# Kernel optimization log

Measured on AMD Instinct MI355X. Metric: run time of the kernel, lower is better.

## Reference

```python
import jax, jax.numpy as jnp
import numpy as np

T, R, H, DK = 2, 3, 4, 32
IN_DIM, OUT_DIM = 128, 128
N = 50000
E = 400000
RELS = [(0, 1), (1, 0), (1, 1)]  # (src_type, dst_type) per relation


def setup_inputs() -> dict:
    key = jax.random.key(0)
    ks = jax.random.split(key, 24)
    lin_scale = float(np.sqrt(2.0 / (IN_DIM + OUT_DIM)))
    att_scale = float(np.sqrt(2.0 / (DK + DK)))
    inp = {
        'h0': jax.random.normal(ks[0], (N, IN_DIM), jnp.float32),
        'h1': jax.random.normal(ks[1], (N, IN_DIM), jnp.float32),
        'Wk': jax.random.normal(ks[2], (T, IN_DIM, OUT_DIM), jnp.float32) * lin_scale,
        'bk': jnp.zeros((T, OUT_DIM), jnp.float32),
        'Wq': jax.random.normal(ks[3], (T, IN_DIM, OUT_DIM), jnp.float32) * lin_scale,
        'bq': jnp.zeros((T, OUT_DIM), jnp.float32),
        'Wv': jax.random.normal(ks[4], (T, IN_DIM, OUT_DIM), jnp.float32) * lin_scale,
        'bv': jnp.zeros((T, OUT_DIM), jnp.float32),
        'Wa': jax.random.normal(ks[5], (T, OUT_DIM, OUT_DIM), jnp.float32) * lin_scale,
        'ba': jnp.zeros((T, OUT_DIM), jnp.float32),
        'rel_att': jax.random.normal(ks[6], (R, H, DK, DK), jnp.float32) * att_scale,
        'rel_msg': jax.random.normal(ks[7], (R, H, DK, DK), jnp.float32) * att_scale,
        'rel_pri': jnp.ones((R, H), jnp.float32),
        'skip': jnp.ones((T,), jnp.float32),
        'src0': jax.random.randint(ks[8], (E,), 0, N, jnp.int32),
        'dst0': jax.random.randint(ks[9], (E,), 0, N, jnp.int32),
        'src1': jax.random.randint(ks[10], (E,), 0, N, jnp.int32),
        'dst1': jax.random.randint(ks[11], (E,), 0, N, jnp.int32),
        'src2': jax.random.randint(ks[12], (E,), 0, N, jnp.int32),
        'dst2': jax.random.randint(ks[13], (E,), 0, N, jnp.int32),
    }
    return inp


def _hgt_forward(h0, h1, Wk, bk, Wq, bq, Wv, bv, Wa, ba,
                 rel_att, rel_msg, rel_pri, skip, edges):
    sqrt_dk = np.sqrt(DK).astype(np.float32)
    hs = [h0, h1]
    # per-type k/q/v projections, reshaped to [N, H, DK]
    k_all = [(hs[t] @ Wk[t] + bk[t]).reshape(-1, H, DK) for t in range(T)]
    q_all = [(hs[t] @ Wq[t] + bq[t]).reshape(-1, H, DK) for t in range(T)]
    v_all = [(hs[t] @ Wv[t] + bv[t]).reshape(-1, H, DK) for t in range(T)]
    agg = {0: [], 1: []}
    for r, (s, d) in enumerate(RELS):
        src, dst = edges[r]
        k = jnp.einsum('nhi,hij->nhj', k_all[s], rel_att[r])
        v = jnp.einsum('nhi,hij->nhj', v_all[s], rel_msg[r])
        q = q_all[d]
        # edge-wise dot-product attention score [E, H]
        score = jnp.einsum('ehd,ehd->eh', q[dst], k[src]) * rel_pri[r] / sqrt_dk
        # edge softmax normalized by destination node
        m = jax.ops.segment_max(score, dst, num_segments=N)
        e = jnp.exp(score - m[dst])
        z = jax.ops.segment_sum(e, dst, num_segments=N)
        a = e / z[dst]
        msg = v[src] * a[..., None]  # [E, H, DK]
        agg[d].append(jax.ops.segment_sum(msg, dst, num_segments=N))
    outs = []
    for t in range(T):
        tmean = agg[t][0]
        for extra in agg[t][1:]:
            tmean = tmean + extra
        tmean = tmean / jnp.float32(len(agg[t]))  # cross_reducer='mean'
        tt = tmean.reshape(-1, OUT_DIM)
        trans = tt @ Wa[t] + ba[t]  # dropout p=0 -> identity
        alpha = jax.nn.sigmoid(skip[t])
        outs.append(trans * alpha + hs[t] * (1.0 - alpha))
    return jnp.stack(outs)  # [T, N, OUT_DIM]


def reference(h0, h1, Wk, bk, Wq, bq, Wv, bv, Wa, ba,
              rel_att, rel_msg, rel_pri, skip,
              src0, dst0, src1, dst1, src2, dst2):
    edges = [(src0, dst0), (src1, dst1), (src2, dst2)]
    return _hgt_forward(h0, h1, Wk, bk, Wq, bq, Wv, bv, Wa, ba,
                        rel_att, rel_msg, rel_pri, skip, edges)
```

## Files before the change

kernel.cpp:

```cpp
#include <hip/hip_runtime.h>
#include <hip/hip_bf16.h>
#include <math.h>


#define NN 50000
#define EE 400000
#define CAP 40
#define NBKT 196
#define SLICE 40

typedef __bf16 bf16x8 __attribute__((ext_vector_type(8)));
typedef float floatx4 __attribute__((ext_vector_type(4)));
typedef _Float16 h2 __attribute__((ext_vector_type(2)));

#if __has_builtin(__builtin_amdgcn_exp2f)
#define EXP2F(x) __builtin_amdgcn_exp2f(x)
#else
#define EXP2F(x) exp2f(x)
#endif

__device__ __forceinline__ h2 u_to_h2(unsigned int u) {
    union { unsigned int u; h2 h; } x; x.u = u; return x.h;
}

__device__ __forceinline__ float dot2f(h2 a, h2 b, float c) {
#if __has_builtin(__builtin_amdgcn_fdot2)
    return __builtin_amdgcn_fdot2(a, b, c, false);
#else
    return fmaf((float)a.x, (float)b.x, fmaf((float)a.y, (float)b.y, c));
#endif
}

__device__ __forceinline__ float xor1_add(float x) {
#if __has_builtin(__builtin_amdgcn_mov_dpp)
    int y = __builtin_amdgcn_mov_dpp(__float_as_int(x), 0xB1, 0xf, 0xf, true);
    return x + __int_as_float(y);
#else
    return x + __shfl_xor(x, 1);
#endif
}
__device__ __forceinline__ float xor2_add(float x) {
#if __has_builtin(__builtin_amdgcn_mov_dpp)
    int y = __builtin_amdgcn_mov_dpp(__float_as_int(x), 0x4E, 0xf, 0xf, true);
    return x + __int_as_float(y);
#else
    return x + __shfl_xor(x, 2);
#endif
}
__device__ __forceinline__ float xor4_add(float x) {
#if __has_builtin(__builtin_amdgcn_ds_swizzle)
    int y = __builtin_amdgcn_ds_swizzle(__float_as_int(x), 0x101F);
    return x + __int_as_float(y);
#else
    return x + __shfl_xor(x, 4);
#endif
}

#define FUSEB 640
__global__ __launch_bounds__(256) void prep(
    const float* __restrict__ Wk, const float* __restrict__ bk,
    const float* __restrict__ Wq, const float* __restrict__ bq,
    const float* __restrict__ Wv, const float* __restrict__ bv,
    const float* __restrict__ rel_att, const float* __restrict__ rel_msg,
    const float* __restrict__ rel_pri, const float* __restrict__ Wa,
    __hip_bfloat16* __restrict__ Wcat0T, __hip_bfloat16* __restrict__ Wcat1T,
    __hip_bfloat16* __restrict__ WaT,
    float* __restrict__ bcat0, float* __restrict__ bcat1,
    const int* __restrict__ s0, const int* __restrict__ d0,
    const int* __restrict__ s1, const int* __restrict__ d1,
    const int* __restrict__ s2, const int* __restrict__ d2,
    int* __restrict__ seg, int* __restrict__ cnt2)
{
    __shared__ int cur[NBKT];
    __shared__ int stage[NBKT * SLICE];
    if (blockIdx.x >= FUSEB) {
        int ab = blockIdx.x - FUSEB;
        int r = ab / NBKT;
        int blk = ab - r * NBKT;
        const int* S = (r == 0) ? s0 : (r == 1) ? s1 : s2;
        const int* D = (r == 0) ? d0 : (r == 1) ? d1 : d2;
        for (int t = threadIdx.x; t < NBKT; t += 256) cur[t] = 0;
        __syncthreads();
        int e0 = blk * 2048 + threadIdx.x * 8;
        if (e0 + 8 <= EE) {
            int sv[8], dv[8];
            *(int4*)&sv[0] = *(const int4*)(S + e0);
            *(int4*)&sv[4] = *(const int4*)(S + e0 + 4);
            *(int4*)&dv[0] = *(const int4*)(D + e0);
            *(int4*)&dv[4] = *(const int4*)(D + e0 + 4);
            #pragma unroll
            for (int j = 0; j < 8; ++j) {
                int d = dv[j];
                int bkt = d >> 8;
                int pos = atomicAdd(&cur[bkt], 1);
                if (pos < SLICE)
                    stage[bkt * SLICE + pos] = sv[j] | ((d & 255) << 16);
            }
        } else {
            for (int j = 0; j < 8; ++j) {
                int e = e0 + j;
                if (e >= EE) break;
                int d = D[e];
                int bkt = d >> 8;
                int pos = atomicAdd(&cur[bkt], 1);
                if (pos < SLICE)
                    stage[bkt * SLICE + pos] = S[e] | ((d & 255) << 16);
            }
        }
        __syncthreads();
        int* gout = seg + (size_t)(r * NBKT + blk) * (NBKT * SLICE);
        const int N4 = (NBKT * SLICE) / 4;
        for (int li = threadIdx.x; li < N4; li += 256)
            ((int4*)gout)[li] = ((const int4*)stage)[li];
        for (int t = threadIdx.x; t < NBKT; t += 256)
            cnt2[((size_t)r * NBKT + blk) * NBKT + t] = min(cur[t], SLICE);
        return;
    }
    int idx = blockIdx.x * 256 + threadIdx.x;
    const int R1 = 128 * 384, R2 = 128 * 640, R3 = 2 * 128 * 128;
    if (idx >= R1 + R2 + R3) return;
    if (idx >= R1 + R2) {
        int t = idx - R1 - R2;
        int tt = t >> 14, rem = t & 16383;
        int k = rem >> 7, col = rem & 127;
        WaT[tt * 16384 + col * 128 + k] = __float2bfloat16(Wa[tt * 16384 + k * 128 + col]);
        return;
    }
    int typ, i, col;
    __hip_bfloat16* Wout; float* bout;
    if (idx < R1) { typ = 0; i = idx / 384; col = idx % 384; Wout = Wcat0T; bout = bcat0; }
    else { idx -= R1; typ = 1; i = idx / 640; col = idx % 640; Wout = Wcat1T; bout = bcat1; }
    float w, b;
    if (col < 128) {
        w = Wq[(typ * 128 + i) * 128 + col];
        b = bq[typ * 128 + col];
    } else {
        int kvcol = col - 128;
        int r = (typ == 0) ? 0 : (1 + (kvcol >> 8));
        int gc = kvcol & 255;
        int isV = (gc >> 2) & 1;
        int c = (gc >> 3) * 4 + (gc & 3);
        int s = typ;
        const float* Wsrc = isV ? Wv : Wk;
        const float* bsrc = isV ? bv : bk;
        const float* rel  = isV ? rel_msg : rel_att;
        int h = c >> 5, j = c & 31;
        float acc = 0.f, bacc = 0.f;
        #pragma unroll
        for (int cc = 0; cc < 32; ++cc) {
            float rr = rel[((r * 4 + h) * 32 + cc) * 32 + j];
            acc  += Wsrc[(s * 128 + i) * 128 + h * 32 + cc] * rr;
            bacc += bsrc[s * 128 + h * 32 + cc] * rr;
        }
        if (!isV) {
            float sc = rel_pri[r * 4 + h] * (0.17677669529663687f * 1.4426950408889634f);
            acc *= sc; bacc *= sc;
        }
        w = acc; b = bacc;
    }
    Wout[col * 128 + i] = __float2bfloat16(w);
    if (i == 0) bout[col] = b;
}

#define SCATX 294
__global__ __launch_bounds__(256) void proj_both(
    const float* __restrict__ h0, const float* __restrict__ h1,
    const __hip_bfloat16* __restrict__ W0T, const __hip_bfloat16* __restrict__ W1T,
    const float* __restrict__ b0, const float* __restrict__ b1,
    ushort* __restrict__ Q0, ushort* __restrict__ Q1,
    ushort* __restrict__ KV0, ushort* __restrict__ KV1,
    ushort* __restrict__ KV2,
    const int* __restrict__ seg, const int* __restrict__ cnt2,
    int* __restrict__ sorted_src, int* __restrict__ counts)
{
    __shared__ __align__(16) char smem[2 * 128 * 136 * 2];
    const int tid = threadIdx.x;

    if (blockIdx.x < SCATX) {
        int pb = blockIdx.y * SCATX + blockIdx.x;
        int r = pb / NBKT;
        int b = pb - r * NBKT;
        int* stage  = (int*)smem;
        int* cntl   = stage + 256 * CAP;
        int* rowcnt = cntl + NBKT;
        if (tid < NBKT) cntl[tid] = cnt2[((size_t)r * NBKT + tid) * NBKT + b];
        rowcnt[tid] = 0;
        int4 z4 = make_int4(0, 0, 0, 0);
        #pragma unroll
        for (int it = 0; it < (256 * CAP) / 4 / 256; ++it)
            ((int4*)stage)[it * 256 + tid] = z4;
        __syncthreads();

        const int* segr = seg + (size_t)r * NBKT * NBKT * SLICE;
        const int NE4 = (NBKT * SLICE) / 4;
        for (int li4 = tid; li4 < NE4; li4 += 256) {
            int e = li4 * 4;
            int s = e / SLICE;
            int k = e - s * SLICE;
            int4 pv = *(const int4*)(segr + ((size_t)s * NBKT + b) * SLICE + k);
            int pvals[4] = { pv.x, pv.y, pv.z, pv.w };
            #pragma unroll
            for (int j = 0; j < 4; ++j) {
                if (k + j < cntl[s]) {
                    int p = pvals[j];
                    int dlow = (unsigned)p >> 16;
                    int srcv = p & 0xFFFF;
                    int pos = atomicAdd(&rowcnt[dlow], 1);
                    if (pos < CAP) stage[dlow * CAP + pos] = srcv;
                }
            }
        }
        __syncthreads();

        int nrows = min(256, NN - b * 256);
        int* gout = sorted_src + ((size_t)r * NN + b * 256) * CAP;
        int n4 = nrows * (CAP / 4);
        for (int li = tid; li < n4; li += 256)
            ((int4*)gout)[li] = ((int4*)stage)[li];
        if (tid < nrows) counts[(size_t)r * NN + b * 256 + tid] = rowcnt[tid];
        return;
    }

    typedef __hip_bfloat16 bfrow[136];
    typedef ushort usrow[136];
    bfrow* As = (bfrow*)smem;
    usrow* Bs = (usrow*)(smem + 128 * 136 * 2);

    const int row0 = (blockIdx.x - SCATX) * 128;
    const int typ = blockIdx.y;
    const float* A = typ ? h1 : h0;
    const __hip_bfloat16* WT = typ ? W1T : W0T;
    const float* bias = typ ? b1 : b0;
    const int ntiles = typ ? 5 : 3;

    #pragma unroll
    for (int it = 0; it < 16; ++it) {
        int li = it * 256 + tid;
        int r = li >> 5, k4 = (li & 31) * 4;
        int grow = row0 + r;
        float4 a4 = make_float4(0.f, 0.f, 0.f, 0.f);
        if (grow < NN) a4 = *(const float4*)(A + (size_t)grow * 128 + k4);
        As[r][k4 + 0] = __float2bfloat16(a4.x);
        As[r][k4 + 1] = __float2bfloat16(a4.y);
        As[r][k4 + 2] = __float2bfloat16(a4.z);
        As[r][k4 + 3] = __float2bfloat16(a4.w);
    }

    const int lane = tid & 63;
    const int wv = tid >> 6;
    const int wr = (wv & 1) * 64, wc = (wv >> 1) * 64;
    const int lr = lane & 15, kq = lane >> 4;

    for (int ct = 0; ct < ntiles; ++ct) {
        __syncthreads();
        #pragma unroll
        for (int it = 0; it < 8; ++it) {
            int li = it * 256 + tid;
            int c = li >> 4, k8 = (li & 15) * 8;
            *(uint4*)&Bs[c][k8] = *(const uint4*)(WT + (size_t)(ct * 128 + c) * 128 + k8);
        }
        __syncthreads();

        floatx4 acc[4][4];
        #pragma unroll
        for (int i = 0; i < 4; ++i)
            #pragma unroll
            for (int j = 0; j < 4; ++j)
                acc[i][j] = (floatx4){0.f, 0.f, 0.f, 0.f};

        #pragma unroll
        for (int kc = 0; kc < 128; kc += 32) {
            bf16x8 a[4], b[4];
            #pragma unroll
            for (int i = 0; i < 4; ++i) a[i] = *(const bf16x8*)&As[wr + i * 16 + lr][kc + kq * 8];
            #pragma unroll
            for (int j = 0; j < 4; ++j) b[j] = *(const bf16x8*)&Bs[wc + j * 16 + lr][kc + kq * 8];
            #pragma unroll
            for (int i = 0; i < 4; ++i)
                #pragma unroll
                for (int j = 0; j < 4; ++j)
                    acc[i][j] = __builtin_amdgcn_mfma_f32_16x16x32_bf16(a[i], b[j], acc[i][j], 0, 0, 0);
        }

        float biasv[4];
        #pragma unroll
        for (int j = 0; j < 4; ++j) biasv[j] = bias[ct * 128 + wc + j * 16 + lr];

        __syncthreads();
        #pragma unroll
        for (int i = 0; i < 4; ++i)
            #pragma unroll
            for (int reg = 0; reg < 4; ++reg) {
                int row = wr + i * 16 + kq * 4 + reg;
                #pragma unroll
                for (int j = 0; j < 4; ++j) {
                    union { _Float16 h; ushort s; } cv;
                    cv.h = (_Float16)(acc[i][j][reg] + biasv[j]);
                    Bs[row][wc + j * 16 + lr] = cv.s;
                }
            }
        __syncthreads();

        ushort* plane; int ld, toff;
        if (ct == 0) { plane = typ ? Q1 : Q0; ld = 128; toff = 0; }
        else {
            int rel = typ ? (1 + ((ct - 1) >> 1)) : 0;
            plane = (rel == 0) ? KV0 : (rel == 1) ? KV1 : KV2;
            ld = 256; toff = ((ct - 1) & 1) * 128;
        }
        #pragma unroll
        for (int it = 0; it < 8; ++it) {
            int li = it * 256 + tid;
            int row = li >> 4, chunk = (li & 15) * 8;
            int grow = row0 + row;
            if (grow < NN)
                *(uint4*)(plane + (size_t)grow * ld + toff + chunk) = *(const uint4*)&Bs[row][chunk];
        }
    }
}

__device__ __forceinline__ void epi_body(
    char* smem,
    const __hip_bfloat16* __restrict__ A0, const __hip_bfloat16* __restrict__ A1, float ascale,
    const __hip_bfloat16* __restrict__ BT, const float* __restrict__ bias,
    float* __restrict__ C, const float* __restrict__ skipGate, const float* __restrict__ Hres)
{
    typedef __hip_bfloat16 bfrow[136];
    bfrow* As = (bfrow*)smem;
    bfrow* Bs = (bfrow*)(smem + 128 * 136 * 2);
    typedef float frow[132];
    frow* St = (frow*)smem;
    const int tid = threadIdx.x;
    const int row0 = blockIdx.x * 128;

    #pragma unroll
    for (int it = 0; it < 8; ++it) {
        int li = it * 256 + tid;
        int c = li >> 4, k8 = (li & 15) * 8;
        *(uint4*)&Bs[c][k8] = *(const uint4*)(BT + (size_t)c * 128 + k8);
    }
    #pragma unroll
    for (int it = 0; it < 8; ++it) {
        int li = it * 256 + tid;
        int r = li >> 4, k8 = (li & 15) * 8;
        int grow = row0 + r;
        __hip_bfloat162 o2[4];
        if (grow < NN) {
            const __hip_bfloat162* pa = (const __hip_bfloat162*)(A0 + (size_t)grow * 128 + k8);
            if (A1) {
                const __hip_bfloat162* pb = (const __hip_bfloat162*)(A1 + (size_t)grow * 128 + k8);
                #pragma unroll
                for (int u = 0; u < 4; ++u) {
                    float2 fa = __bfloat1622float2(pa[u]);
                    float2 fb = __bfloat1622float2(pb[u]);
                    fa.x = (fa.x + fb.x) * ascale;
                    fa.y = (fa.y + fb.y) * ascale;
                    o2[u] = __float22bfloat162_rn(fa);
                }
            } else {
                #pragma unroll
                for (int u = 0; u < 4; ++u) o2[u] = pa[u];
            }
        } else {
            __hip_bfloat162 zz = __float22bfloat162_rn(make_float2(0.f, 0.f));
            #pragma unroll
            for (int u = 0; u < 4; ++u) o2[u] = zz;
        }
        __hip_bfloat162* dst = (__hip_bfloat162*)&As[r][k8];
        #pragma unroll
        for (int u = 0; u < 4; ++u) dst[u] = o2[u];
    }
    __syncthreads();

    const int lane = tid & 63;
    const int wv = tid >> 6;
    const int wr = (wv & 1) * 64, wc = (wv >> 1) * 64;
    const int lr = lane & 15, kq = lane >> 4;

    floatx4 acc[4][4];
    #pragma unroll
    for (int i = 0; i < 4; ++i)
        #pragma unroll
        for (int j = 0; j < 4; ++j)
            acc[i][j] = (floatx4){0.f, 0.f, 0.f, 0.f};

    #pragma unroll
    for (int kc = 0; kc < 128; kc += 32) {
        bf16x8 a[4], b[4];
        #pragma unroll
        for (int i = 0; i < 4; ++i) a[i] = *(const bf16x8*)&As[wr + i * 16 + lr][kc + kq * 8];
        #pragma unroll
        for (int j = 0; j < 4; ++j) b[j] = *(const bf16x8*)&Bs[wc + j * 16 + lr][kc + kq * 8];
        #pragma unroll
        for (int i = 0; i < 4; ++i)
            #pragma unroll
            for (int j = 0; j < 4; ++j)
                acc[i][j] = __builtin_amdgcn_mfma_f32_16x16x32_bf16(a[i], b[j], acc[i][j], 0, 0, 0);
    }

    float sg = *skipGate;
    float alpha = 1.f / (1.f + expf(-sg));
    float beta = 1.f - alpha;
    float biasv[4];
    #pragma unroll
    for (int j = 0; j < 4; ++j) biasv[j] = bias[wc + j * 16 + lr];

    __syncthreads();
    #pragma unroll
    for (int i = 0; i < 4; ++i)
        #pragma unroll
        for (int reg = 0; reg < 4; ++reg) {
            int row = wr + i * 16 + kq * 4 + reg;
            #pragma unroll
            for (int j = 0; j < 4; ++j)
                St[row][wc + j * 16 + lr] = acc[i][j][reg] + biasv[j];
        }
    __syncthreads();

    #pragma unroll
    for (int it = 0; it < 16; ++it) {
        int li = it * 256 + tid;
        int row = li >> 5, chunk = (li & 31) * 4;
        int grow = row0 + row;
        if (grow < NN) {
            float4 v = *(const float4*)&St[row][chunk];
            float4 hr = *(const float4*)(Hres + (size_t)grow * 128 + chunk);
            v.x = v.x * alpha + hr.x * beta;
            v.y = v.y * alpha + hr.y * beta;
            v.z = v.z * alpha + hr.z * beta;
            v.w = v.w * alpha + hr.w * beta;
            *(float4*)(C + (size_t)grow * 128 + chunk) = v;
        }
    }
}

__global__ __launch_bounds__(256) void epi_both(
    const __hip_bfloat16* __restrict__ aggR0, const __hip_bfloat16* __restrict__ aggR1,
    const __hip_bfloat16* __restrict__ aggR2,
    const __hip_bfloat16* __restrict__ WaT, const float* __restrict__ ba,
    float* __restrict__ out, const float* __restrict__ skip,
    const float* __restrict__ h0, const float* __restrict__ h1)
{
    __shared__ __align__(16) char smem[128 * 136 * 2 * 2];
    if (blockIdx.y == 0)
        epi_body(smem, aggR1, nullptr, 1.f, WaT, ba, out, skip, h0);
    else
        epi_body(smem, aggR0, aggR2, 0.5f, WaT + 16384, ba + 128,
                 out + (size_t)NN * 128, skip + 1, h1);
}

__device__ __forceinline__ void edge4_accum(
    uint4 ra, uint4 rb, uint4 rc, uint4 rd,
    bool mA, bool mB, bool mC, bool mD,
    h2 q01, h2 q23,
    float& z, float& u0, float& u1, float& u2, float& u3)
{
    float pa = dot2f(u_to_h2(ra.x), q01, 0.f); pa = dot2f(u_to_h2(ra.y), q23, pa);
    float pb = dot2f(u_to_h2(rb.x), q01, 0.f); pb = dot2f(u_to_h2(rb.y), q23, pb);
    float pc = dot2f(u_to_h2(rc.x), q01, 0.f); pc = dot2f(u_to_h2(rc.y), q23, pc);
    float pd = dot2f(u_to_h2(rd.x), q01, 0.f); pd = dot2f(u_to_h2(rd.y), q23, pd);
    pa = xor1_add(pa); pb = xor1_add(pb); pc = xor1_add(pc); pd = xor1_add(pd);
    pa = xor2_add(pa); pb = xor2_add(pb); pc = xor2_add(pc); pd = xor2_add(pd);
    pa = xor4_add(pa); pb = xor4_add(pb); pc = xor4_add(pc); pd = xor4_add(pd);
    float ea = EXP2F(pa); if (!mA) ea = 0.f;
    float eb = EXP2F(pb); if (!mB) eb = 0.f;
    float ec = EXP2F(pc); if (!mC) ec = 0.f;
    float ed = EXP2F(pd); if (!mD) ed = 0.f;
    z += (ea + eb) + (ec + ed);
    h2 va, vb;
    va = u_to_h2(ra.z); vb = u_to_h2(ra.w);
    u0 = fmaf(ea, (float)va.x, u0); u1 = fmaf(ea, (float)va.y, u1);
    u2 = fmaf(ea, (float)vb.x, u2); u3 = fmaf(ea, (float)vb.y, u3);
    va = u_to_h2(rb.z); vb = u_to_h2(rb.w);
    u0 = fmaf(eb, (float)va.x, u0); u1 = fmaf(eb, (float)va.y, u1);
    u2 = fmaf(eb, (float)vb.x, u2); u3 = fmaf(eb, (float)vb.y, u3);
    va = u_to_h2(rc.z); vb = u_to_h2(rc.w);
    u0 = fmaf(ec, (float)va.x, u0); u1 = fmaf(ec, (float)va.y, u1);
    u2 = fmaf(ec, (float)vb.x, u2); u3 = fmaf(ec, (float)vb.y, u3);
    va = u_to_h2(rd.z); vb = u_to_h2(rd.w);
    u0 = fmaf(ed, (float)va.x, u0); u1 = fmaf(ed, (float)va.y, u1);
    u2 = fmaf(ed, (float)vb.x, u2); u3 = fmaf(ed, (float)vb.y, u3);
}

__global__ __launch_bounds__(256) void aggregate_all(
    const ushort* __restrict__ Q0, const ushort* __restrict__ Q1,
    const ushort* __restrict__ KV0, const ushort* __restrict__ KV1,
    const ushort* __restrict__ KV2,
    const int* __restrict__ sorted, const int* __restrict__ counts,
    __hip_bfloat16* __restrict__ aggR0, __hip_bfloat16* __restrict__ aggR1,
    __hip_bfloat16* __restrict__ aggR2)
{
    int n = (blockIdx.x * 256 + threadIdx.x) >> 6;
    int lane = threadIdx.x & 63;
    int r = blockIdx.y;
    const ushort *Q, *KV; __hip_bfloat16* outp;
    if (r == 0)      { Q = Q1; KV = KV0; outp = aggR0; }
    else if (r == 1) { Q = Q0; KV = KV1; outp = aggR1; }
    else             { Q = Q1; KV = KV2; outp = aggR2; }
    int gw = r * NN + n;

    int hl = lane & 31;
    int half = lane >> 5;

    int cnt = min(counts[gw], CAP);
    uint2 qr = *(const uint2*)(Q + (size_t)n * 128 + hl * 4);
    const int* elist = sorted + (size_t)gw * CAP;
    int4 v0 = *(const int4*)elist;
    int4 v1 = *(const int4*)(elist + 4);
    int4 v2 = *(const int4*)(elist + 8);
    int4 v3 = *(const int4*)(elist + 12);

    int i0 = half ? v0.y : v0.x;
    int i1 = half ? v0.w : v0.z;
    int i2 = half ? v1.y : v1.x;
    int i3 = half ? v1.w : v1.z;
    int j0 = half ? v2.y : v2.x;
    int j1 = half ? v2.w : v2.z;
    int j2 = half ? v3.y : v3.x;
    int j3 = half ? v3.w : v3.z;
    uint4 ra = *(const uint4*)(KV + (size_t)(unsigned)(i0 * 256 + hl * 8));
    uint4 rb = *(const uint4*)(KV + (size_t)(unsigned)(i1 * 256 + hl * 8));
    uint4 rc = *(const uint4*)(KV + (size_t)(unsigned)(i2 * 256 + hl * 8));
    uint4 rd = *(const uint4*)(KV + (size_t)(unsigned)(i3 * 256 + hl * 8));

    h2 q01 = u_to_h2(qr.x), q23 = u_to_h2(qr.y);

    bool mA = (0 + half) < cnt, mB = (2 + half) < cnt, mC = (4 + half) < cnt, mD = (6 + half) < cnt;
    float u0 = 0.f, u1 = 0.f, u2 = 0.f, u3 = 0.f, z = 0.f;
    edge4_accum(ra, rb, rc, rd, mA, mB, mC, mD, q01, q23, z, u0, u1, u2, u3);

    if (cnt > 8) {
        uint4 sa = *(const uint4*)(KV + (size_t)(unsigned)(j0 * 256 + hl * 8));
        uint4 sb = *(const uint4*)(KV + (size_t)(unsigned)(j1 * 256 + hl * 8));
        uint4 sc = *(const uint4*)(KV + (size_t)(unsigned)(j2 * 256 + hl * 8));
        uint4 sd = *(const uint4*)(KV + (size_t)(unsigned)(j3 * 256 + hl * 8));
        bool nA = (8 + half) < cnt, nB = (10 + half) < cnt, nC = (12 + half) < cnt, nD = (14 + half) < cnt;
        edge4_accum(sa, sb, sc, sd, nA, nB, nC, nD, q01, q23, z, u0, u1, u2, u3);

        for (int i = 16; i < cnt; i += 4) {
            int eA = i + half, eB = i + 2 + half;
            int sA = elist[min(eA, cnt - 1)];
            int sB = elist[min(eB, cnt - 1)];
            uint4 ta = *(const uint4*)(KV + (size_t)(unsigned)(sA * 256 + hl * 8));
            uint4 tb = *(const uint4*)(KV + (size_t)(unsigned)(sB * 256 + hl * 8));
            float pa = dot2f(u_to_h2(ta.x), q01, 0.f); pa = dot2f(u_to_h2(ta.y), q23, pa);
            float pb = dot2f(u_to_h2(tb.x), q01, 0.f); pb = dot2f(u_to_h2(tb.y), q23, pb);
            pa = xor1_add(pa); pb = xor1_add(pb);
            pa = xor2_add(pa); pb = xor2_add(pb);
            pa = xor4_add(pa); pb = xor4_add(pb);
            float ea = EXP2F(pa);
            float eb = EXP2F(pb);
            if (eA >= cnt) ea = 0.f;
            if (eB >= cnt) eb = 0.f;
            z += ea + eb;
            h2 va = u_to_h2(ta.z), vb = u_to_h2(ta.w);
            u0 = fmaf(ea, (float)va.x, u0); u1 = fmaf(ea, (float)va.y, u1);
            u2 = fmaf(ea, (float)vb.x, u2); u3 = fmaf(ea, (float)vb.y, u3);
            va = u_to_h2(tb.z); vb = u_to_h2(tb.w);
            u0 = fmaf(eb, (float)va.x, u0); u1 = fmaf(eb, (float)va.y, u1);
            u2 = fmaf(eb, (float)vb.x, u2); u3 = fmaf(eb, (float)vb.y, u3);
        }
    }

    z  += __shfl_xor(z, 32);
    u0 += __shfl_xor(u0, 32);
    u1 += __shfl_xor(u1, 32);
    u2 += __shfl_xor(u2, 32);
    u3 += __shfl_xor(u3, 32);
    if (half == 0) {
        float inv = (cnt > 0) ? 1.f / z : 0.f;
        __hip_bfloat162 o0 = __float22bfloat162_rn(make_float2(u0 * inv, u1 * inv));
        __hip_bfloat162 o1 = __float22bfloat162_rn(make_float2(u2 * inv, u3 * inv));
        union { uint2 u; __hip_bfloat162 h[2]; } pk2;
        pk2.h[0] = o0; pk2.h[1] = o1;
        *(uint2*)(outp + (size_t)n * 128 + hl * 4) = pk2.u;
    }
}

extern "C" void kernel_launch(void* const* d_in, const int* in_sizes, int n_in,
                              void* d_out, int out_size, void* d_ws, size_t ws_size,
                              hipStream_t stream)
{
    const float* h0      = (const float*)d_in[0];
    const float* h1      = (const float*)d_in[1];
    const float* Wk      = (const float*)d_in[2];
    const float* bk      = (const float*)d_in[3];
    const float* Wq      = (const float*)d_in[4];
    const float* bq      = (const float*)d_in[5];
    const float* Wv      = (const float*)d_in[6];
    const float* bv      = (const float*)d_in[7];
    const float* Wa      = (const float*)d_in[8];
    const float* ba      = (const float*)d_in[9];
    const float* rel_att = (const float*)d_in[10];
    const float* rel_msg = (const float*)d_in[11];
    const float* rel_pri = (const float*)d_in[12];
    const float* skip    = (const float*)d_in[13];
    const int*   src0    = (const int*)d_in[14];
    const int*   dst0    = (const int*)d_in[15];
    const int*   src1    = (const int*)d_in[16];
    const int*   dst1    = (const int*)d_in[17];
    const int*   src2    = (const int*)d_in[18];
    const int*   dst2    = (const int*)d_in[19];
    float* out = (float*)d_out;

    char* w = (char*)d_ws;
    auto alloc = [&](size_t bytes) -> char* {
        char* p = w; w += (bytes + 255) & ~(size_t)255; return p;
    };
    __hip_bfloat16* Wcat0T = (__hip_bfloat16*)alloc(384 * 128 * 2);
    __hip_bfloat16* Wcat1T = (__hip_bfloat16*)alloc(640 * 128 * 2);
    __hip_bfloat16* WaT    = (__hip_bfloat16*)alloc(2 * 128 * 128 * 2);
    float* bcat0 = (float*)alloc(384 * sizeof(float));
    float* bcat1 = (float*)alloc(640 * sizeof(float));
    ushort* Q0  = (ushort*)alloc((size_t)NN * 128 * 2);
    ushort* Q1  = (ushort*)alloc((size_t)NN * 128 * 2);
    ushort* KV0 = (ushort*)alloc((size_t)NN * 256 * 2);
    ushort* KV1 = (ushort*)alloc((size_t)NN * 256 * 2);
    ushort* KV2 = (ushort*)alloc((size_t)NN * 256 * 2);
    __hip_bfloat16* aggR0 = (__hip_bfloat16*)alloc((size_t)NN * 128 * 2);
    __hip_bfloat16* aggR1 = (__hip_bfloat16*)alloc((size_t)NN * 128 * 2);
    __hip_bfloat16* aggR2 = (__hip_bfloat16*)alloc((size_t)NN * 128 * 2);
    int* counts  = (int*)alloc(3 * NN * sizeof(int));
    int* sorted  = (int*)alloc((size_t)3 * NN * CAP * sizeof(int));

    int* seg  = (int*)aggR0;
    int* cnt2 = seg + (size_t)3 * NBKT * NBKT * SLICE;

    if ((size_t)(w - (char*)d_ws) > ws_size) return;

    prep<<<FUSEB + 3 * NBKT, 256, 0, stream>>>(
        Wk, bk, Wq, bq, Wv, bv, rel_att, rel_msg, rel_pri, Wa,
        Wcat0T, Wcat1T, WaT, bcat0, bcat1,
        src0, dst0, src1, dst1, src2, dst2, seg, cnt2);

    const int ROWB = (NN + 127) / 128;
    proj_both<<<dim3(SCATX + ROWB, 2), 256, 0, stream>>>(
        h0, h1, Wcat0T, Wcat1T, bcat0, bcat1,
        Q0, Q1, KV0, KV1, KV2,
        seg, cnt2, sorted, counts);

    const int AG = (NN * 64) / 256;
    aggregate_all<<<dim3(AG, 3), 256, 0, stream>>>(Q0, Q1, KV0, KV1, KV2, sorted, counts,
                                                   aggR0, aggR1, aggR2);

    epi_both<<<dim3(ROWB, 2), 256, 0, stream>>>(aggR0, aggR1, aggR2, WaT, ba, out, skip, h0, h1);
}
```

Measured before the change: 312.4 us.

## Store sorted edge lists as ushort and map one half-wave per node

The per-destination sorted source lists are now stored as 16-bit indices instead of 32-bit, which halves the CSR write in the scatter stage and the read in aggregation. Aggregation now gives each half-wave its own destination node rather than splitting one node's edges across two halves, so the cross-half shuffle reduction goes away and the grid shrinks by half. Each half-wave loads 8 edges up front, which adds more gathers in flight per thread and more registers. This relies on source indices fitting in 16 bits, which they do here only through the low-16 bucket packing.

```diff
diff --git a/kernel.cpp b/kernel.cpp
--- a/kernel.cpp
+++ b/kernel.cpp
@@ -171,7 +171,7 @@
     ushort* __restrict__ KV0, ushort* __restrict__ KV1,
     ushort* __restrict__ KV2,
     const int* __restrict__ seg, const int* __restrict__ cnt2,
-    int* __restrict__ sorted_src, int* __restrict__ counts)
+    ushort* __restrict__ sorted_src, int* __restrict__ counts)
 {
     __shared__ __align__(16) char smem[2 * 128 * 136 * 2];
     const int tid = threadIdx.x;
@@ -180,15 +180,15 @@
         int pb = blockIdx.y * SCATX + blockIdx.x;
         int r = pb / NBKT;
         int b = pb - r * NBKT;
-        int* stage  = (int*)smem;
-        int* cntl   = stage + 256 * CAP;
+        ushort* stageu = (ushort*)smem;
+        int* cntl   = (int*)(smem + 256 * CAP * 2);
         int* rowcnt = cntl + NBKT;
         if (tid < NBKT) cntl[tid] = cnt2[((size_t)r * NBKT + tid) * NBKT + b];
         rowcnt[tid] = 0;
         int4 z4 = make_int4(0, 0, 0, 0);
         #pragma unroll
-        for (int it = 0; it < (256 * CAP) / 4 / 256; ++it)
-            ((int4*)stage)[it * 256 + tid] = z4;
+        for (int it = 0; it < (256 * CAP * 2) / 16 / 256; ++it)
+            ((int4*)stageu)[it * 256 + tid] = z4;
         __syncthreads();
 
         const int* segr = seg + (size_t)r * NBKT * NBKT * SLICE;
@@ -206,17 +206,17 @@
                     int dlow = (unsigned)p >> 16;
                     int srcv = p & 0xFFFF;
                     int pos = atomicAdd(&rowcnt[dlow], 1);
-                    if (pos < CAP) stage[dlow * CAP + pos] = srcv;
+                    if (pos < CAP) stageu[dlow * CAP + pos] = (ushort)srcv;
                 }
             }
         }
         __syncthreads();
 
         int nrows = min(256, NN - b * 256);
-        int* gout = sorted_src + ((size_t)r * NN + b * 256) * CAP;
-        int n4 = nrows * (CAP / 4);
+        ushort* gout = sorted_src + ((size_t)r * NN + b * 256) * CAP;
+        int n4 = nrows * 5;
         for (int li = tid; li < n4; li += 256)
-            ((int4*)gout)[li] = ((int4*)stage)[li];
+            ((int4*)gout)[li] = ((int4*)stageu)[li];
         if (tid < nrows) counts[(size_t)r * NN + b * 256 + tid] = rowcnt[tid];
         return;
     }
@@ -486,12 +486,15 @@
     const ushort* __restrict__ Q0, const ushort* __restrict__ Q1,
     const ushort* __restrict__ KV0, const ushort* __restrict__ KV1,
     const ushort* __restrict__ KV2,
-    const int* __restrict__ sorted, const int* __restrict__ counts,
+    const ushort* __restrict__ sorted, const int* __restrict__ counts,
     __hip_bfloat16* __restrict__ aggR0, __hip_bfloat16* __restrict__ aggR1,
     __hip_bfloat16* __restrict__ aggR2)
 {
-    int n = (blockIdx.x * 256 + threadIdx.x) >> 6;
+    int wid = blockIdx.x * 4 + (threadIdx.x >> 6);
     int lane = threadIdx.x & 63;
+    int half = lane >> 5;
+    int hl = lane & 31;
+    int n = wid * 2 + half;
     int r = blockIdx.y;
     const ushort *Q, *KV; __hip_bfloat16* outp;
     if (r == 0)      { Q = Q1; KV = KV0; outp = aggR0; }
@@ -499,48 +502,54 @@
     else             { Q = Q1; KV = KV2; outp = aggR2; }
     int gw = r * NN + n;
 
-    int hl = lane & 31;
-    int half = lane >> 5;
-
     int cnt = min(counts[gw], CAP);
     uint2 qr = *(const uint2*)(Q + (size_t)n * 128 + hl * 4);
-    const int* elist = sorted + (size_t)gw * CAP;
-    int4 v0 = *(const int4*)elist;
-    int4 v1 = *(const int4*)(elist + 4);
-    int4 v2 = *(const int4*)(elist + 8);
-    int4 v3 = *(const int4*)(elist + 12);
-
-    int i0 = half ? v0.y : v0.x;
-    int i1 = half ? v0.w : v0.z;
-    int i2 = half ? v1.y : v1.x;
-    int i3 = half ? v1.w : v1.z;
-    int j0 = half ? v2.y : v2.x;
-    int j1 = half ? v2.w : v2.z;
-    int j2 = half ? v3.y : v3.x;
-    int j3 = half ? v3.w : v3.z;
-    uint4 ra = *(const uint4*)(KV + (size_t)(unsigned)(i0 * 256 + hl * 8));
-    uint4 rb = *(const uint4*)(KV + (size_t)(unsigned)(i1 * 256 + hl * 8));
-    uint4 rc = *(const uint4*)(KV + (size_t)(unsigned)(i2 * 256 + hl * 8));
-    uint4 rd = *(const uint4*)(KV + (size_t)(unsigned)(i3 * 256 + hl * 8));
+    const ushort* elist = sorted + (size_t)gw * CAP;
+    uint4 ev  = *(const uint4*)elist;
+    uint4 ev2 = *(const uint4*)(elist + 8);
+
+    int e0 = ev.x & 0xFFFF, e1 = (int)(ev.x >> 16);
+    int e2 = ev.y & 0xFFFF, e3 = (int)(ev.y >> 16);
+    int e4 = ev.z & 0xFFFF, e5 = (int)(ev.z >> 16);
+    int e6 = ev.w & 0xFFFF, e7 = (int)(ev.w >> 16);
+    uint4 r0 = *(const uint4*)(KV + (size_t)(unsigned)(e0 * 256 + hl * 8));
+    uint4 r1 = *(const uint4*)(KV + (size_t)(unsigned)(e1 * 256 + hl * 8));
+    uint4 r2 = *(const uint4*)(KV + (size_t)(unsigned)(e2 * 256 + hl * 8));
+    uint4 r3 = *(const uint4*)(KV + (size_t)(unsigned)(e3 * 256 + hl * 8));
+    uint4 r4 = *(const uint4*)(KV + (size_t)(unsigned)(e4 * 256 + hl * 8));
+    uint4 r5 = *(const uint4*)(KV + (size_t)(unsigned)(e5 * 256 + hl * 8));
+    uint4 r6 = *(const uint4*)(KV + (size_t)(unsigned)(e6 * 256 + hl * 8));
+    uint4 r7 = *(const uint4*)(KV + (size_t)(unsigned)(e7 * 256 + hl * 8));
 
     h2 q01 = u_to_h2(qr.x), q23 = u_to_h2(qr.y);
 
-    bool mA = (0 + half) < cnt, mB = (2 + half) < cnt, mC = (4 + half) < cnt, mD = (6 + half) < cnt;
     float u0 = 0.f, u1 = 0.f, u2 = 0.f, u3 = 0.f, z = 0.f;
-    edge4_accum(ra, rb, rc, rd, mA, mB, mC, mD, q01, q23, z, u0, u1, u2, u3);
+    edge4_accum(r0, r1, r2, r3, 0 < cnt, 1 < cnt, 2 < cnt, 3 < cnt,
+                q01, q23, z, u0, u1, u2, u3);
+    edge4_accum(r4, r5, r6, r7, 4 < cnt, 5 < cnt, 6 < cnt, 7 < cnt,
+                q01, q23, z, u0, u1, u2, u3);
 
     if (cnt > 8) {
-        uint4 sa = *(const uint4*)(KV + (size_t)(unsigned)(j0 * 256 + hl * 8));
-        uint4 sb = *(const uint4*)(KV + (size_t)(unsigned)(j1 * 256 + hl * 8));
-        uint4 sc = *(const uint4*)(KV + (size_t)(unsigned)(j2 * 256 + hl * 8));
-        uint4 sd = *(const uint4*)(KV + (size_t)(unsigned)(j3 * 256 + hl * 8));
-        bool nA = (8 + half) < cnt, nB = (10 + half) < cnt, nC = (12 + half) < cnt, nD = (14 + half) < cnt;
-        edge4_accum(sa, sb, sc, sd, nA, nB, nC, nD, q01, q23, z, u0, u1, u2, u3);
-
-        for (int i = 16; i < cnt; i += 4) {
-            int eA = i + half, eB = i + 2 + half;
-            int sA = elist[min(eA, cnt - 1)];
-            int sB = elist[min(eB, cnt - 1)];
+        int f0 = ev2.x & 0xFFFF, f1 = (int)(ev2.x >> 16);
+        int f2 = ev2.y & 0xFFFF, f3 = (int)(ev2.y >> 16);
+        int f4 = ev2.z & 0xFFFF, f5 = (int)(ev2.z >> 16);
+        int f6 = ev2.w & 0xFFFF, f7 = (int)(ev2.w >> 16);
+        uint4 s0 = *(const uint4*)(KV + (size_t)(unsigned)(f0 * 256 + hl * 8));
+        uint4 s1 = *(const uint4*)(KV + (size_t)(unsigned)(f1 * 256 + hl * 8));
+        uint4 s2 = *(const uint4*)(KV + (size_t)(unsigned)(f2 * 256 + hl * 8));
+        uint4 s3 = *(const uint4*)(KV + (size_t)(unsigned)(f3 * 256 + hl * 8));
+        uint4 s4 = *(const uint4*)(KV + (size_t)(unsigned)(f4 * 256 + hl * 8));
+        uint4 s5 = *(const uint4*)(KV + (size_t)(unsigned)(f5 * 256 + hl * 8));
+        uint4 s6 = *(const uint4*)(KV + (size_t)(unsigned)(f6 * 256 + hl * 8));
+        uint4 s7 = *(const uint4*)(KV + (size_t)(unsigned)(f7 * 256 + hl * 8));
+        edge4_accum(s0, s1, s2, s3, 8 < cnt, 9 < cnt, 10 < cnt, 11 < cnt,
+                    q01, q23, z, u0, u1, u2, u3);
+        edge4_accum(s4, s5, s6, s7, 12 < cnt, 13 < cnt, 14 < cnt, 15 < cnt,
+                    q01, q23, z, u0, u1, u2, u3);
+
+        for (int i = 16; i < cnt; i += 2) {
+            int sA = elist[i];
+            int sB = elist[min(i + 1, cnt - 1)];
             uint4 ta = *(const uint4*)(KV + (size_t)(unsigned)(sA * 256 + hl * 8));
             uint4 tb = *(const uint4*)(KV + (size_t)(unsigned)(sB * 256 + hl * 8));
             float pa = dot2f(u_to_h2(ta.x), q01, 0.f); pa = dot2f(u_to_h2(ta.y), q23, pa);
@@ -550,8 +559,7 @@
             pa = xor4_add(pa); pb = xor4_add(pb);
             float ea = EXP2F(pa);
             float eb = EXP2F(pb);
-            if (eA >= cnt) ea = 0.f;
-            if (eB >= cnt) eb = 0.f;
+            if (i + 1 >= cnt) eb = 0.f;
             z += ea + eb;
             h2 va = u_to_h2(ta.z), vb = u_to_h2(ta.w);
             u0 = fmaf(ea, (float)va.x, u0); u1 = fmaf(ea, (float)va.y, u1);
@@ -562,19 +570,12 @@
         }
     }
 
-    z  += __shfl_xor(z, 32);
-    u0 += __shfl_xor(u0, 32);
-    u1 += __shfl_xor(u1, 32);
-    u2 += __shfl_xor(u2, 32);
-    u3 += __shfl_xor(u3, 32);
-    if (half == 0) {
-        float inv = (cnt > 0) ? 1.f / z : 0.f;
-        __hip_bfloat162 o0 = __float22bfloat162_rn(make_float2(u0 * inv, u1 * inv));
-        __hip_bfloat162 o1 = __float22bfloat162_rn(make_float2(u2 * inv, u3 * inv));
-        union { uint2 u; __hip_bfloat162 h[2]; } pk2;
-        pk2.h[0] = o0; pk2.h[1] = o1;
-        *(uint2*)(outp + (size_t)n * 128 + hl * 4) = pk2.u;
-    }
+    float inv = (cnt > 0) ? 1.f / z : 0.f;
+    __hip_bfloat162 o0 = __float22bfloat162_rn(make_float2(u0 * inv, u1 * inv));
+    __hip_bfloat162 o1 = __float22bfloat162_rn(make_float2(u2 * inv, u3 * inv));
+    union { uint2 u; __hip_bfloat162 h[2]; } pk2;
+    pk2.h[0] = o0; pk2.h[1] = o1;
+    *(uint2*)(outp + (size_t)n * 128 + hl * 4) = pk2.u;
 }
 
 extern "C" void kernel_launch(void* const* d_in, const int* in_sizes, int n_in,
@@ -621,7 +622,7 @@
     __hip_bfloat16* aggR1 = (__hip_bfloat16*)alloc((size_t)NN * 128 * 2);
     __hip_bfloat16* aggR2 = (__hip_bfloat16*)alloc((size_t)NN * 128 * 2);
     int* counts  = (int*)alloc(3 * NN * sizeof(int));
-    int* sorted  = (int*)alloc((size_t)3 * NN * CAP * sizeof(int));
+    ushort* sorted = (ushort*)alloc((size_t)3 * NN * CAP * sizeof(ushort));
 
     int* seg  = (int*)aggR0;
     int* cnt2 = seg + (size_t)3 * NBKT * NBKT * SLICE;
@@ -639,7 +640,7 @@
         Q0, Q1, KV0, KV1, KV2,
         seg, cnt2, sorted, counts);
 
-    const int AG = (NN * 64) / 256;
+    const int AG = NN / 8;
     aggregate_all<<<dim3(AG, 3), 256, 0, stream>>>(Q0, Q1, KV0, KV1, KV2, sorted, counts,
                                                    aggR0, aggR1, aggR2);
 
```

Result: no change. 311.4 us (-0.3%).
